# Kernel tuning notes

Hardware: AMD Instinct MI355X
Metric: run time of the kernel (lower is better)

The kernel has to match this reference:

```python
import jax, jax.numpy as jnp
import numpy as np
from jax import lax

SCALE = 2
K_UP = 5
BN_EPS = 1e-5
DN = ('NCHW', 'OIHW', 'NCHW')


def bn_eval(x, gamma, beta):
    # BatchNorm2d in eval mode with running_mean=0, running_var=1
    s = gamma / jnp.sqrt(1.0 + BN_EPS)
    return x * s[None, :, None, None] + beta[None, :, None, None]


def pixel_shuffle(x, r):
    b, C, h, w = x.shape
    c = C // (r * r)
    x = x.reshape(b, c, r, r, h, w)
    x = x.transpose(0, 1, 4, 2, 5, 3)  # b, c, h, r, w, r
    return x.reshape(b, c, h * r, w * r)


def setup_inputs() -> dict:
    key = jax.random.key(0)
    ks = jax.random.split(key, 3)
    b, c, h, w = 4, 128, 64, 64
    c_mid = 64
    return {
        'X': jax.random.normal(ks[0], (b, c, h, w), dtype=jnp.float32),
        'comp_w': jax.random.normal(ks[1], (c_mid, c, 1, 1), dtype=jnp.float32) * 0.05,
        'comp_g': jnp.ones((c_mid,), jnp.float32),
        'comp_b': jnp.zeros((c_mid,), jnp.float32),
        'enc_w': jax.random.normal(ks[2], ((SCALE * K_UP) ** 2, c_mid, 3, 3), dtype=jnp.float32) * 0.05,
        'enc_g': jnp.ones(((SCALE * K_UP) ** 2,), jnp.float32),
        'enc_b': jnp.zeros(((SCALE * K_UP) ** 2,), jnp.float32),
    }


def reference(X, comp_w, comp_g, comp_b, enc_w, enc_g, enc_b):
    b, c, h, w = X.shape
    h_, w_ = h * SCALE, w * SCALE
    pad = K_UP // 2 * SCALE  # = 4

    # comp: 1x1 conv + BN + SiLU
    W = lax.conv_general_dilated(X, comp_w, (1, 1), [(0, 0), (0, 0)], dimension_numbers=DN)
    W = jax.nn.silu(bn_eval(W, comp_g, comp_b))
    # enc: 3x3 conv (pad 1) + BN, no activation
    W = lax.conv_general_dilated(W, enc_w, (1, 1), [(1, 1), (1, 1)], dimension_numbers=DN)
    W = bn_eval(W, enc_g, enc_b)
    # pixel shuffle -> [b, k_up^2, h_, w_], softmax over kernel dim
    W = pixel_shuffle(W, SCALE)
    W = jax.nn.softmax(W, axis=1)

    # nearest-neighbor upsample of X
    Xu = jnp.repeat(jnp.repeat(X, SCALE, axis=2), SCALE, axis=3)  # [b, c, h_, w_]
    # unfold: kernel k_up, dilation=scale, padding=pad (im2col, channel-major)
    P = lax.conv_general_dilated_patches(
        Xu, (K_UP, K_UP), (1, 1), [(pad, pad), (pad, pad)],
        rhs_dilation=(SCALE, SCALE), dimension_numbers=DN)  # [b, c*k^2, h_, w_]
    P = P.reshape(b, c, K_UP * K_UP, h_, w_)

    return jnp.einsum('bkhw,bckhw->bchw', W, P)
```

## Files before the change

### kernel.cpp

```cpp
#include <hip/hip_runtime.h>
#include <hip/hip_bf16.h>
#include <math.h>

#define Bn   4
#define CIN  128
#define Hh   64
#define Ww   64
#define HW   4096
#define CMID 64
#define KOC  100
#define H2   128
#define W2d  128
#define HW2  16384
#define KUP  5
#define BN_EPS 1e-5f
#define CCH  8

typedef __attribute__((ext_vector_type(4)))  short  short4v;
typedef __attribute__((ext_vector_type(8)))  short  short8v;
typedef __attribute__((ext_vector_type(16))) float  float16v;

__device__ __forceinline__ ushort f2bf(float v) {
    __hip_bfloat16 h = __float2bfloat16(v);
    return *(ushort*)&h;
}

__global__ __launch_bounds__(256) void comp_kernel(
    const float* __restrict__ X,
    const float* __restrict__ cw,
    const float* __restrict__ cg,
    const float* __restrict__ cb,
    const float* __restrict__ ew,
    ushort* __restrict__ W1b,
    ushort* __restrict__ Abf)
{
    __shared__ float cwS[64 * 129];

    int tid = threadIdx.x;
    int blk = blockIdx.x;

    for (int i = tid; i < 64 * 128; i += 256) {
        int co_s = i >> 7, ci_s = i & 127;
        cwS[co_s * 129 + ci_s] = cw[i];
    }

    if (blk < 288) {
        int i   = blk * 256 + tid;
        int cm  = i & 63;
        int kop = (i >> 6) & 127;
        int tap = i >> 13;
        float v = (kop < KOC) ? ew[((size_t)(kop * CMID + cm)) * 9 + tap] : 0.f;
        Abf[i] = f2bf(v);
    }
    __syncthreads();

    int b   = blk >> 8;
    int pix = ((blk & 255) << 4) + ((tid >> 6) << 2);
    int co  = tid & 63;

    const float* xb = X + (size_t)b * CIN * HW + pix;
    const float* wrow = cwS + co * 129;
    float a0 = 0.f, a1 = 0.f, a2 = 0.f, a3 = 0.f;

#pragma unroll 4
    for (int ci = 0; ci < CIN; ++ci) {
        float4 xv = *(const float4*)(xb + (size_t)ci * HW);
        float w = wrow[ci];
        a0 += xv.x * w; a1 += xv.y * w; a2 += xv.z * w; a3 += xv.w * w;
    }

    float inv_s = rsqrtf(1.0f + BN_EPS);
    float s0 = cg[co] * inv_s, bb0 = cb[co];
    float r[4] = {a0, a1, a2, a3};
    ushort* wp = W1b + ((size_t)b * HW + pix) * 64 + co;
#pragma unroll
    for (int i = 0; i < 4; ++i) {
        float v = r[i] * s0 + bb0;
        v = v / (1.f + expf(-v));
        wp[(size_t)i * 64] = f2bf(v);
    }
}

__global__ __launch_bounds__(256) void enc_kernel(
    const ushort* __restrict__ W1b_us,
    const ushort* __restrict__ Abf,
    const float* __restrict__ eg,
    const float* __restrict__ eb,
    float* __restrict__ Wsm)
{
    __shared__ ushort Bs[3 * 34 * 72];
    __shared__ float  redm[4][8][32];
    __shared__ float  reds[4][8][32];

    int bid   = blockIdx.x;
    int whalf = bid & 1;
    int h     = (bid >> 1) & 63;
    int b     = bid >> 7;
    int w0    = whalf * 32;
    int tid   = threadIdx.x;

    const unsigned* src  = (const unsigned*)W1b_us;
    unsigned*       dstu = (unsigned*)Bs;
    for (int i = tid; i < 3 * 34 * 32; i += 256) {
        int cp = i & 31;
        int t  = i >> 5;
        int wl = t % 34;
        int r  = t / 34;
        int gr = h - 1 + r, gw = w0 - 1 + wl;
        unsigned val = 0u;
        if ((unsigned)gr < 64u && (unsigned)gw < 64u)
            val = src[((size_t)b * HW + gr * 64 + gw) * 32 + cp];
        dstu[(r * 34 + wl) * 36 + cp] = val;
    }
    __syncthreads();

    int lane = tid & 63;
    int wid  = tid >> 6;
    int n    = lane & 31;
    int q    = lane >> 5;

    float16v acc;
#pragma unroll
    for (int i = 0; i < 16; ++i) acc[i] = 0.f;

    const ushort* Arow = Abf + ((size_t)(wid * 32 + n)) * 64 + q * 8;

#pragma unroll
    for (int tap = 0; tap < 9; ++tap) {
        int dy = tap / 3, dx = tap % 3;
        int bbase = ((dy * 34) + n + dx) * 72 + q * 8;
        const ushort* Atap = Arow + (size_t)tap * 128 * 64;
#pragma unroll
        for (int c = 0; c < 4; ++c) {
            short8v a = *(const short8v*)(Atap + c * 16);
            short8v bf = *(const short8v*)(Bs + bbase + c * 16);
            acc = __builtin_amdgcn_mfma_f32_32x32x16_bf16(a, bf, acc, 0, 0, 0);
        }
    }

    float inv_s = rsqrtf(1.0f + BN_EPS);
    int   widq  = wid * 2 + q;

    float v[16];
    float pmax[4] = {-1e30f, -1e30f, -1e30f, -1e30f};
#pragma unroll
    for (int g = 0; g < 4; ++g) {
        int base = wid * 32 + 8 * g + 4 * q;
        if (base < KOC) {
            float4 gg = *(const float4*)(eg + base);
            float4 bb = *(const float4*)(eb + base);
            float v0 = acc[4*g+0] * (gg.x * inv_s) + bb.x;
            float v1 = acc[4*g+1] * (gg.y * inv_s) + bb.y;
            float v2 = acc[4*g+2] * (gg.z * inv_s) + bb.z;
            float v3 = acc[4*g+3] * (gg.w * inv_s) + bb.w;
            v[4*g+0] = v0; v[4*g+1] = v1; v[4*g+2] = v2; v[4*g+3] = v3;
            pmax[0] = fmaxf(pmax[0], v0);
            pmax[1] = fmaxf(pmax[1], v1);
            pmax[2] = fmaxf(pmax[2], v2);
            pmax[3] = fmaxf(pmax[3], v3);
        } else {
            v[4*g+0] = -1e30f; v[4*g+1] = -1e30f;
            v[4*g+2] = -1e30f; v[4*g+3] = -1e30f;
        }
    }

#pragma unroll
    for (int j = 0; j < 4; ++j) redm[j][widq][n] = pmax[j];
    __syncthreads();
    float m[4];
#pragma unroll
    for (int j = 0; j < 4; ++j) {
        float mm = redm[j][0][n];
#pragma unroll
        for (int i = 1; i < 8; ++i) mm = fmaxf(mm, redm[j][i][n]);
        m[j] = mm;
    }

    float psum[4] = {0.f, 0.f, 0.f, 0.f};
#pragma unroll
    for (int g = 0; g < 4; ++g) {
#pragma unroll
        for (int j = 0; j < 4; ++j) {
            float e = expf(v[4*g+j] - m[j]);
            v[4*g+j] = e;
            psum[j] += e;
        }
    }
#pragma unroll
    for (int j = 0; j < 4; ++j) reds[j][widq][n] = psum[j];
    __syncthreads();
    float inv[4];
#pragma unroll
    for (int j = 0; j < 4; ++j) {
        float ss = reds[j][0][n];
#pragma unroll
        for (int i = 1; i < 8; ++i) ss += reds[j][i][n];
        inv[j] = 1.f / ss;
    }

    int pixn = h * 64 + w0 + n;
    float* Wp = Wsm + (size_t)b * KOC * HW + pixn;
#pragma unroll
    for (int reg = 0; reg < 16; ++reg) {
        int row = (reg & 3) + 8 * (reg >> 2) + 4 * q;
        int ko  = wid * 32 + row;
        if (ko < KOC) Wp[(size_t)ko * HW] = v[reg] * inv[reg & 3];
    }
}

__global__ __launch_bounds__(256) void carafe_kernel(
    const float* __restrict__ X,
    const float* __restrict__ Wsm,
    float* __restrict__ out)
{
    int gt = blockIdx.x * blockDim.x + threadIdx.x;
    int w  = gt & 63;
    int h  = (gt >> 6) & 63;
    int b  = (gt >> 12) & 3;
    int chunk = gt >> 14;
    int c0 = chunk * CCH;
    int pix = h * Ww + w;

    float wt[100];
    const float* wpb = Wsm + (size_t)b * KOC * HW + pix;
#pragma unroll
    for (int k = 0; k < 25; ++k) {
        wt[k]      = wpb[(size_t)(4 * k + 0) * HW];
        wt[25 + k] = wpb[(size_t)(4 * k + 1) * HW];
        wt[50 + k] = wpb[(size_t)(4 * k + 2) * HW];
        wt[75 + k] = wpb[(size_t)(4 * k + 3) * HW];
    }

    int off[25];
#pragma unroll
    for (int ki = 0; ki < 5; ++ki) {
#pragma unroll
        for (int kj = 0; kj < 5; ++kj) {
            int k = ki * 5 + kj;
            int r = h + ki - 2, cc = w + kj - 2;
            bool valid = ((unsigned)r < 64u) && ((unsigned)cc < 64u);
            int rc = r < 0 ? 0 : (r > 63 ? 63 : r);
            int cx = cc < 0 ? 0 : (cc > 63 ? 63 : cc);
            off[k] = rc * Ww + cx;
            if (!valid) { wt[k] = 0.f; wt[25+k] = 0.f; wt[50+k] = 0.f; wt[75+k] = 0.f; }
        }
    }

    const float* xp = X + ((size_t)b * CIN + c0) * HW;
    float* o0 = out + ((size_t)b * CIN + c0) * HW2 + (2 * h) * W2d + 2 * w;

    for (int c = 0; c < CCH; ++c) {
        float x[25];
#pragma unroll
        for (int k = 0; k < 25; ++k) x[k] = xp[off[k]];
        float a0 = 0.f, a1 = 0.f, a2 = 0.f, a3 = 0.f;
#pragma unroll
        for (int k = 0; k < 25; ++k) {
            float xv = x[k];
            a0 += wt[k]      * xv;
            a1 += wt[25 + k] * xv;
            a2 += wt[50 + k] * xv;
            a3 += wt[75 + k] * xv;
        }
        *(float2*)o0          = make_float2(a0, a1);
        *(float2*)(o0 + W2d)  = make_float2(a2, a3);
        xp += HW;
        o0 += HW2;
    }
}

extern "C" void kernel_launch(void* const* d_in, const int* in_sizes, int n_in,
                              void* d_out, int out_size, void* d_ws, size_t ws_size,
                              hipStream_t stream)
{
    const float* X  = (const float*)d_in[0];
    const float* cw = (const float*)d_in[1];
    const float* cg = (const float*)d_in[2];
    const float* cb = (const float*)d_in[3];
    const float* ew = (const float*)d_in[4];
    const float* eg = (const float*)d_in[5];
    const float* eb = (const float*)d_in[6];
    float* out = (float*)d_out;

    char* ws = (char*)d_ws;
    ushort* W1b = (ushort*)ws;
    ushort* Abf = (ushort*)(ws + 2097152);
    float*  Wsm = (float*)(ws + 2097152 + 147456);

    comp_kernel  <<<1024, 256, 0, stream>>>(X, cw, cg, cb, ew, W1b, Abf);
    enc_kernel   <<<512, 256, 0, stream>>>(W1b, Abf, eg, eb, Wsm);
    carafe_kernel<<<16 * Bn * HW / 256, 256, 0, stream>>>(X, Wsm, out);
}
```

Baseline: 128.1 us.

## Compute 1x1 comp conv with split-bf16 MFMA instead of scalar FMA

```diff
diff --git a/kernel.cpp b/kernel.cpp
--- a/kernel.cpp
+++ b/kernel.cpp
@@ -18,11 +18,16 @@
 
 typedef __attribute__((ext_vector_type(4)))  short  short4v;
 typedef __attribute__((ext_vector_type(8)))  short  short8v;
+typedef __attribute__((ext_vector_type(4)))  float  float4v;
 typedef __attribute__((ext_vector_type(16))) float  float16v;
 
 __device__ __forceinline__ ushort f2bf(float v) {
     __hip_bfloat16 h = __float2bfloat16(v);
     return *(ushort*)&h;
+}
+__device__ __forceinline__ float bfbits2f(ushort u) {
+    unsigned x = ((unsigned)u) << 16;
+    return __uint_as_float(x);
 }
 
 __global__ __launch_bounds__(256) void comp_kernel(
@@ -34,51 +39,79 @@
     ushort* __restrict__ W1b,
     ushort* __restrict__ Abf)
 {
-    __shared__ float cwS[64 * 129];
-
     int tid = threadIdx.x;
-    int blk = blockIdx.x;
-
-    for (int i = tid; i < 64 * 128; i += 256) {
-        int co_s = i >> 7, ci_s = i & 127;
-        cwS[co_s * 129 + ci_s] = cw[i];
-    }
-
-    if (blk < 288) {
-        int i   = blk * 256 + tid;
+    int bid = blockIdx.x;
+
+    if (tid < 72) {
+        int i   = bid * 72 + tid;
         int cm  = i & 63;
         int kop = (i >> 6) & 127;
         int tap = i >> 13;
         float v = (kop < KOC) ? ew[((size_t)(kop * CMID + cm)) * 9 + tap] : 0.f;
         Abf[i] = f2bf(v);
     }
-    __syncthreads();
-
-    int b   = blk >> 8;
-    int pix = ((blk & 255) << 4) + ((tid >> 6) << 2);
-    int co  = tid & 63;
-
-    const float* xb = X + (size_t)b * CIN * HW + pix;
-    const float* wrow = cwS + co * 129;
-    float a0 = 0.f, a1 = 0.f, a2 = 0.f, a3 = 0.f;
-
-#pragma unroll 4
-    for (int ci = 0; ci < CIN; ++ci) {
-        float4 xv = *(const float4*)(xb + (size_t)ci * HW);
-        float w = wrow[ci];
-        a0 += xv.x * w; a1 += xv.y * w; a2 += xv.z * w; a3 += xv.w * w;
+
+    int b    = bid >> 8;
+    int rem  = bid & 255;
+    int pixG = rem >> 1;
+    int coH  = rem & 1;
+
+    int lane = tid & 63;
+    int wid  = tid >> 6;
+    int i16  = lane & 15;
+    int u    = lane >> 4;
+
+    int co0  = coH * 32 + (wid >> 1) * 16;
+    int pix  = pixG * 32 + (wid & 1) * 16 + i16;
+
+    const float* xcol = X  + (size_t)b * CIN * HW + pix;
+    const float* arow = cw + (size_t)(co0 + i16) * CIN;
+
+    float4v acc;
+    acc[0] = 0.f; acc[1] = 0.f; acc[2] = 0.f; acc[3] = 0.f;
+
+#pragma unroll
+    for (int c = 0; c < 4; ++c) {
+        int k0 = c * 32 + u * 8;
+        float4 wa0 = *(const float4*)(arow + k0);
+        float4 wa1 = *(const float4*)(arow + k0 + 4);
+        float wv[8] = {wa0.x, wa0.y, wa0.z, wa0.w, wa1.x, wa1.y, wa1.z, wa1.w};
+        float xv[8];
+#pragma unroll
+        for (int e = 0; e < 8; ++e)
+            xv[e] = xcol[(size_t)(k0 + e) * HW];
+
+        short8v ah, al, bh, bl;
+#pragma unroll
+        for (int e = 0; e < 8; ++e) {
+            ushort h = f2bf(wv[e]);
+            ah[e] = (short)h;
+            al[e] = (short)f2bf(wv[e] - bfbits2f(h));
+            ushort xh = f2bf(xv[e]);
+            bh[e] = (short)xh;
+            bl[e] = (short)f2bf(xv[e] - bfbits2f(xh));
+        }
+        acc = __builtin_amdgcn_mfma_f32_16x16x32_bf16(ah, bh, acc, 0, 0, 0);
+        acc = __builtin_amdgcn_mfma_f32_16x16x32_bf16(ah, bl, acc, 0, 0, 0);
+        acc = __builtin_amdgcn_mfma_f32_16x16x32_bf16(al, bh, acc, 0, 0, 0);
     }
 
     float inv_s = rsqrtf(1.0f + BN_EPS);
-    float s0 = cg[co] * inv_s, bb0 = cb[co];
-    float r[4] = {a0, a1, a2, a3};
-    ushort* wp = W1b + ((size_t)b * HW + pix) * 64 + co;
-#pragma unroll
-    for (int i = 0; i < 4; ++i) {
-        float v = r[i] * s0 + bb0;
-        v = v / (1.f + expf(-v));
-        wp[(size_t)i * 64] = f2bf(v);
-    }
+    int cob = co0 + u * 4;
+    float4 gg = *(const float4*)(cg + cob);
+    float4 bb = *(const float4*)(cb + cob);
+    float v0 = acc[0] * (gg.x * inv_s) + bb.x;
+    float v1 = acc[1] * (gg.y * inv_s) + bb.y;
+    float v2 = acc[2] * (gg.z * inv_s) + bb.z;
+    float v3 = acc[3] * (gg.w * inv_s) + bb.w;
+    v0 = v0 / (1.f + expf(-v0));
+    v1 = v1 / (1.f + expf(-v1));
+    v2 = v2 / (1.f + expf(-v2));
+    v3 = v3 / (1.f + expf(-v3));
+    short4v pk;
+    pk[0] = (short)f2bf(v0); pk[1] = (short)f2bf(v1);
+    pk[2] = (short)f2bf(v2); pk[3] = (short)f2bf(v3);
+    *(short4v*)(W1b + ((size_t)b * HW + pix) * 64 + cob) = pk;
 }
 
 __global__ __launch_bounds__(256) void enc_kernel(
```

New measurement: 117.1 us (median of 2 runs). 1.09x faster.
